# Kernel tuning notes

Measured on AMD Instinct MI355X. Metric: run time of the kernel, lower is better.

Reference implementation:

```python
import jax, jax.numpy as jnp
import numpy as np

DT = 0.1
N_STEPS = 20
STEP_SIZE = DT / N_STEPS


def setup_inputs() -> dict:
    key = jax.random.key(0)
    ks = jax.random.split(key, 8)
    sizes = [1024, 2048, 2048, 10]
    batch = 4096
    inp = {
        "x": jax.random.uniform(ks[0], (batch, sizes[0]), dtype=jnp.float32),
        "w0": jax.random.normal(ks[1], (sizes[0], sizes[1]), dtype=jnp.float32) / np.sqrt(sizes[0]),
        "w1": jax.random.normal(ks[2], (sizes[1], sizes[2]), dtype=jnp.float32) / np.sqrt(sizes[1]),
        "w2": jax.random.normal(ks[3], (sizes[2], sizes[3]), dtype=jnp.float32) / np.sqrt(sizes[2]),
        "b0": jnp.zeros((sizes[1],), jnp.float32),
        "b1": jnp.zeros((sizes[2],), jnp.float32),
        "b2": jnp.zeros((sizes[3],), jnp.float32),
        "s1": jax.random.uniform(ks[4], (batch, sizes[1]), dtype=jnp.float32),
        "s2": jax.random.uniform(ks[5], (batch, sizes[2]), dtype=jnp.float32),
        "s3": jax.random.uniform(ks[6], (batch, sizes[3]), dtype=jnp.float32),
    }
    return inp


def reference(x, w0, w1, w2, b0, b1, b2, s1, s2, s3):
    weights = [w0, w1, w2]
    biases = [b0, b1, b2]
    sig = jax.nn.sigmoid

    def dsig(v):
        s = sig(v)
        return s * (1.0 - s)

    def body(states, _):
        st = list(states)  # [s0(=x, clamped), s1, s2, s3]
        # hidden layers (indices 1..len-2), sequential in-place semantics
        for i in range(1, 3):
            pre = sig(st[i - 1]) @ weights[i - 1] + sig(st[i + 1]) @ weights[i].T + biases[i - 1]
            grad = dsig(st[i]) * pre - st[i]
            st[i] = st[i] - STEP_SIZE * grad
        # output layer (no target / beta=0 in eval mode)
        grad = dsig(st[3]) * (sig(st[2]) @ weights[2] + biases[2]) - st[3]
        st[3] = st[3] - STEP_SIZE * grad
        return tuple(st), None

    init = (x, s1, s2, s3)
    final, _ = jax.lax.scan(body, init, None, length=N_STEPS)
    return final[-1]
```

## Files before the change

### kernel.cpp

```cpp
#include <hip/hip_runtime.h>
#include <cstdint>
#include <cstddef>

using u16 = unsigned short;
using u32 = unsigned int;

typedef __bf16 bf16x8 __attribute__((ext_vector_type(8)));
typedef float f32x4 __attribute__((ext_vector_type(4)));
typedef u16 u16x4 __attribute__((ext_vector_type(4)));

#define DEV __device__ __forceinline__

constexpr float SS = 0.1f / 20.0f;

DEV float sigm(float x) { return 1.0f / (1.0f + __expf(-x)); }

DEV u16 f2bf(float f) {
  union { float f; u32 u; } v; v.f = f;
  u32 r = v.u + 0x7FFFu + ((v.u >> 16) & 1u);
  return (u16)(r >> 16);
}
DEV float bf2f(u16 h) {
  union { u32 u; float f; } v; v.u = ((u32)h) << 16;
  return v.f;
}

__global__ void k_prep(const float* __restrict__ in, float* __restrict__ fcopy,
                       float* __restrict__ sigf32, u16* __restrict__ sigb,
                       u16* __restrict__ rawb, int n) {
  int stride = gridDim.x * blockDim.x;
  for (int i = blockIdx.x * blockDim.x + threadIdx.x; i < n; i += stride) {
    float v = in[i];
    if (fcopy) fcopy[i] = v;
    if (rawb) rawb[i] = f2bf(v);
    if (sigf32 || sigb) {
      float s = sigm(v);
      if (sigf32) sigf32[i] = s;
      if (sigb) sigb[i] = f2bf(s);
    }
  }
}

__global__ void k_transpose_bf16(const float* __restrict__ in, u16* __restrict__ out,
                                 int K, int N) {
  __shared__ float tile[32][33];
  int kb = blockIdx.x * 32, nb = blockIdx.y * 32;
  int tx = threadIdx.x & 31, ty = threadIdx.x >> 5;
#pragma unroll
  for (int i = 0; i < 4; ++i)
    tile[ty + 8 * i][tx] = in[(size_t)(kb + ty + 8 * i) * N + nb + tx];
  __syncthreads();
#pragma unroll
  for (int i = 0; i < 4; ++i)
    out[(size_t)(nb + ty + 8 * i) * K + kb + tx] = f2bf(tile[tx][ty + 8 * i]);
}

template <int MODE>
__launch_bounds__(256)
__global__ void k_gemm(const u16* __restrict__ A, const u16* __restrict__ Bt,
                       int M, int N, int K,
                       const u16* __restrict__ addcb, const float* __restrict__ bias,
                       const float* __restrict__ sig3, const float* __restrict__ w2,
                       float* __restrict__ statef, u16* __restrict__ sigb) {
  constexpr int BM = 128, BN = 128, BK = 64;
  __shared__ __align__(16) u16 Als[2][BM * BK];
  __shared__ __align__(16) u16 Bls[2][BN * BK];
  int b = blockIdx.x;
  int xcd = b & 7, slot = b >> 3;
  int tm = ((((xcd >> 1) << 3) | (slot >> 3))) * BM;
  int tn = ((((xcd & 1) << 3) | (slot & 7))) * BN;
  int tid = threadIdx.x;
  int lane = tid & 63, wid = tid >> 6;
  int l15 = lane & 15, lhi = lane >> 4;
  int wm = (wid >> 1) * 64, wn = (wid & 1) * 64;

  const u16* Ag = A + (size_t)tm * K;
  const u16* Bg = Bt + (size_t)tn * K;

  f32x4 acc[4][4] = {};

  auto stage = [&](int buf, int k0) {
#pragma unroll
    for (int rd = 0; rd < 4; ++rd) {
      int S = rd * 256 + tid;
      int row = S >> 3;
      int cs = ((S & 7) ^ (row & 7)) * 8;
      __builtin_amdgcn_global_load_lds(
          (const __attribute__((address_space(1))) u32*)(Ag + (size_t)row * K + k0 + cs),
          (__attribute__((address_space(3))) u32*)(&Als[buf][0] + S * 8), 16, 0, 0);
      __builtin_amdgcn_global_load_lds(
          (const __attribute__((address_space(1))) u32*)(Bg + (size_t)row * K + k0 + cs),
          (__attribute__((address_space(3))) u32*)(&Bls[buf][0] + S * 8), 16, 0, 0);
    }
  };

  auto compute = [&](int buf) {
    __builtin_amdgcn_s_setprio(1);
#pragma unroll
    for (int s = 0; s < 2; ++s) {
      bf16x8 af[4], bfr[4];
#pragma unroll
      for (int i = 0; i < 4; ++i) {
        int row = wm + i * 16 + l15;
        af[i] = *(const bf16x8*)(&Als[buf][0] + row * BK + (((s * 4 + lhi) ^ (row & 7)) * 8));
      }
#pragma unroll
      for (int j = 0; j < 4; ++j) {
        int row = wn + j * 16 + l15;
        bfr[j] = *(const bf16x8*)(&Bls[buf][0] + row * BK + (((s * 4 + lhi) ^ (row & 7)) * 8));
      }
#pragma unroll
      for (int i = 0; i < 4; ++i)
#pragma unroll
        for (int j = 0; j < 4; ++j)
          acc[i][j] = __builtin_amdgcn_mfma_f32_16x16x32_bf16(bfr[j], af[i], acc[i][j], 0, 0, 0);
    }
    __builtin_amdgcn_s_setprio(0);
  };

  const int nt = K / BK;
  stage(0, 0);
  stage(1, BK);
  asm volatile("s_waitcnt vmcnt(8)" ::: "memory");
  __builtin_amdgcn_s_barrier();
  asm volatile("" ::: "memory");

  int t = 0;
  for (; t + 3 < nt; t += 2) {
    compute(0);
    asm volatile("" ::: "memory");
    __builtin_amdgcn_s_barrier();
    asm volatile("" ::: "memory");
    stage(0, (t + 2) * BK);
    asm volatile("s_waitcnt vmcnt(8)" ::: "memory");
    __builtin_amdgcn_s_barrier();
    asm volatile("" ::: "memory");

    compute(1);
    asm volatile("" ::: "memory");
    __builtin_amdgcn_s_barrier();
    asm volatile("" ::: "memory");
    stage(1, (t + 3) * BK);
    asm volatile("s_waitcnt vmcnt(8)" ::: "memory");
    __builtin_amdgcn_s_barrier();
    asm volatile("" ::: "memory");
  }
  compute(0);
  asm volatile("s_waitcnt vmcnt(0)" ::: "memory");
  __builtin_amdgcn_s_barrier();
  asm volatile("" ::: "memory");
  compute(1);

  if constexpr (MODE == 0) {
#pragma unroll
    for (int i = 0; i < 4; ++i) {
      int gr = tm + wm + i * 16 + l15;
#pragma unroll
      for (int j = 0; j < 4; ++j) {
        int gc0 = tn + wn + j * 16 + 4 * lhi;
        u16x4 sb;
#pragma unroll
        for (int rr = 0; rr < 4; ++rr) sb[rr] = f2bf(acc[i][j][rr] + bias[gc0 + rr]);
        *(u16x4*)(sigb + (size_t)gr * N + gc0) = sb;
      }
    }
  } else if constexpr (MODE == 1) {
#pragma unroll
    for (int i = 0; i < 4; ++i) {
      int gr = tm + wm + i * 16 + l15;
#pragma unroll
      for (int j = 0; j < 4; ++j) {
        int gc0 = tn + wn + j * 16 + 4 * lhi;
        size_t idx = (size_t)gr * N + gc0;
        u16x4 ab = *(const u16x4*)(addcb + idx);
        f32x4 old = *(const f32x4*)(statef + idx);
        f32x4 nv; u16x4 sb;
#pragma unroll
        for (int rr = 0; rr < 4; ++rr) {
          float pre = acc[i][j][rr] + bf2f(ab[rr]);
          float o = old[rr];
          float sg = sigm(o);
          float n = o - SS * (sg * (1.0f - sg) * pre - o);
          nv[rr] = n; sb[rr] = f2bf(sigm(n));
        }
        *(f32x4*)(statef + idx) = nv;
        *(u16x4*)(sigb + idx) = sb;
      }
    }
  } else {
    float s3v[4][10];
#pragma unroll
    for (int i = 0; i < 4; ++i) {
      int gr = tm + wm + i * 16 + l15;
#pragma unroll
      for (int k = 0; k < 10; ++k) s3v[i][k] = sig3[gr * 10 + k];
    }
#pragma unroll
    for (int j = 0; j < 4; ++j) {
      int gc0 = tn + wn + j * 16 + 4 * lhi;
      float wv[4][10]; f32x4 bb;
#pragma unroll
      for (int rr = 0; rr < 4; ++rr) {
        bb[rr] = bias[gc0 + rr];
#pragma unroll
        for (int k = 0; k < 10; ++k) wv[rr][k] = w2[(gc0 + rr) * 10 + k];
      }
#pragma unroll
      for (int i = 0; i < 4; ++i) {
        int gr = tm + wm + i * 16 + l15;
        size_t idx = (size_t)gr * N + gc0;
        f32x4 old = *(const f32x4*)(statef + idx);
        f32x4 nv; u16x4 sb;
#pragma unroll
        for (int rr = 0; rr < 4; ++rr) {
          float ex = bb[rr];
#pragma unroll
          for (int k = 0; k < 10; ++k) ex += s3v[i][k] * wv[rr][k];
          float pre = acc[i][j][rr] + ex;
          float o = old[rr];
          float sg = sigm(o);
          float n = o - SS * (sg * (1.0f - sg) * pre - o);
          nv[rr] = n; sb[rr] = f2bf(sigm(n));
        }
        *(f32x4*)(statef + idx) = nv;
        *(u16x4*)(sigb + idx) = sb;
      }
    }
  }
}

__global__ void k_out(const u16* __restrict__ sigs2b, const float* __restrict__ w2,
                      const float* __restrict__ b2, float* __restrict__ s3f,
                      float* __restrict__ sigs3f, float* __restrict__ outOrNull) {
  int tid = threadIdx.x;
  int r = tid >> 4, l16 = tid & 15;
  int row = blockIdx.x * 16 + r;
  float acc[10] = {};
  const u16* arow = sigs2b + (size_t)row * 2048;
  for (int kb = l16; kb < 256; kb += 16) {
    u16x4 v0 = *(const u16x4*)(arow + kb * 8);
    u16x4 v1 = *(const u16x4*)(arow + kb * 8 + 4);
    float a[8];
#pragma unroll
    for (int e = 0; e < 4; ++e) { a[e] = bf2f(v0[e]); a[e + 4] = bf2f(v1[e]); }
    const float* wr = w2 + (size_t)kb * 80;
#pragma unroll
    for (int e = 0; e < 8; ++e)
#pragma unroll
      for (int n = 0; n < 10; ++n) acc[n] += a[e] * wr[e * 10 + n];
  }
#pragma unroll
  for (int m = 1; m < 16; m <<= 1)
#pragma unroll
    for (int n = 0; n < 10; ++n) acc[n] += __shfl_xor(acc[n], m, 64);
  if (l16 < 10) {
    float pre = 0.0f;
#pragma unroll
    for (int n = 0; n < 10; ++n)
      if (l16 == n) pre = acc[n];
    pre += b2[l16];
    size_t idx = (size_t)row * 10 + l16;
    float old = s3f[idx];
    float sg = sigm(old);
    float nv = old - SS * (sg * (1.0f - sg) * pre - old);
    s3f[idx] = nv;
    sigs3f[idx] = sigm(nv);
    if (outOrNull) outOrNull[idx] = nv;
  }
}

extern "C" void kernel_launch(void* const* d_in, const int* in_sizes, int n_in,
                              void* d_out, int out_size, void* d_ws, size_t ws_size,
                              hipStream_t stream) {
  const float* x  = (const float*)d_in[0];
  const float* w0 = (const float*)d_in[1];
  const float* w1 = (const float*)d_in[2];
  const float* w2 = (const float*)d_in[3];
  const float* b0 = (const float*)d_in[4];
  const float* b1 = (const float*)d_in[5];
  const float* b2 = (const float*)d_in[6];
  const float* s1 = (const float*)d_in[7];
  const float* s2 = (const float*)d_in[8];
  const float* s3 = (const float*)d_in[9];
  float* out = (float*)d_out;

  uint8_t* p = (uint8_t*)d_ws;
  auto alloc = [&](size_t bytes) {
    uint8_t* r = p;
    p += (bytes + 255) & ~(size_t)255;
    return r;
  };
  float* s1f    = (float*)alloc(4096ull * 2048 * 4);
  float* s2f    = (float*)alloc(4096ull * 2048 * 4);
  u16*   addcb  = (u16*)alloc(4096ull * 2048 * 2);
  u16*   sigs1b = (u16*)alloc(4096ull * 2048 * 2);
  u16*   sigs2b = (u16*)alloc(4096ull * 2048 * 2);
  u16*   sigxb  = (u16*)alloc(4096ull * 1024 * 2);
  u16*   w1b    = (u16*)alloc(2048ull * 2048 * 2);
  u16*   w1tb   = (u16*)alloc(2048ull * 2048 * 2);
  u16*   w0tb   = (u16*)alloc(2048ull * 1024 * 2);
  float* s3f    = (float*)alloc(4096ull * 10 * 4);
  float* sigs3f = (float*)alloc(4096ull * 10 * 4);
  (void)ws_size; (void)in_sizes; (void)n_in; (void)out_size;

  auto grid = [](int n) { int g = (n + 255) / 256; return g > 2048 ? 2048 : g; };

  k_prep<<<grid(4096 * 1024), 256, 0, stream>>>(x, nullptr, nullptr, sigxb, nullptr, 4096 * 1024);
  k_prep<<<grid(2048 * 2048), 256, 0, stream>>>(w1, nullptr, nullptr, nullptr, w1b, 2048 * 2048);
  k_prep<<<grid(4096 * 2048), 256, 0, stream>>>(s1, s1f, nullptr, nullptr, nullptr, 4096 * 2048);
  k_prep<<<grid(4096 * 2048), 256, 0, stream>>>(s2, s2f, nullptr, sigs2b, nullptr, 4096 * 2048);
  k_prep<<<grid(40960), 256, 0, stream>>>(s3, s3f, sigs3f, nullptr, nullptr, 40960);
  k_transpose_bf16<<<dim3(1024 / 32, 2048 / 32), 256, 0, stream>>>(w0, w0tb, 1024, 2048);
  k_transpose_bf16<<<dim3(2048 / 32, 2048 / 32), 256, 0, stream>>>(w1, w1tb, 2048, 2048);

  k_gemm<0><<<512, 256, 0, stream>>>(sigxb, w0tb, 4096, 2048, 1024,
                                     nullptr, b0, nullptr, nullptr, nullptr, addcb);

  for (int t = 0; t < 20; ++t) {
    k_gemm<1><<<512, 256, 0, stream>>>(sigs2b, w1b, 4096, 2048, 2048,
                                       addcb, nullptr, nullptr, nullptr, s1f, sigs1b);
    k_gemm<2><<<512, 256, 0, stream>>>(sigs1b, w1tb, 4096, 2048, 2048,
                                       nullptr, b1, sigs3f, w2, s2f, sigs2b);
    k_out<<<256, 256, 0, stream>>>(sigs2b, w2, b2, s3f, sigs3f, (t == 19) ? out : nullptr);
  }
}
```

Measured before the change: 2.521 ms.

## Use 8-wave GEMM blocks and store fp32 state in per-thread swizzled layout

```diff
diff --git a/kernel.cpp b/kernel.cpp
--- a/kernel.cpp
+++ b/kernel.cpp
@@ -55,8 +55,31 @@
     out[(size_t)(nb + ty + 8 * i) * K + kb + tx] = f2bf(tile[tx][ty + 8 * i]);
 }
 
+DEV void tile_base(int b, int& tm, int& tn) {
+  int xcd = b & 7, slot = b >> 3;
+  tm = ((((xcd >> 1) << 3) | (slot >> 3))) * 128;
+  tn = ((((xcd & 1) << 3) | (slot & 7))) * 128;
+}
+
+__global__ void k_init_state(const float* __restrict__ src, float* __restrict__ dst_swz) {
+  int b = blockIdx.x;
+  int tm, tn; tile_base(b, tm, tn);
+  int tid = threadIdx.x, lane = tid & 63, wid = tid >> 6;
+  int l15 = lane & 15, lhi = lane >> 4;
+  int wm = (wid >> 2) * 64, wn = (wid & 3) * 32;
+#pragma unroll
+  for (int i = 0; i < 4; ++i)
+#pragma unroll
+    for (int j = 0; j < 2; ++j) {
+      int gr = tm + wm + i * 16 + l15;
+      int gc0 = tn + wn + j * 16 + 4 * lhi;
+      f32x4 v = *(const f32x4*)(src + (size_t)gr * 2048 + gc0);
+      *(f32x4*)(dst_swz + (((size_t)b * 8 + i * 2 + j) * 512 + tid) * 4) = v;
+    }
+}
+
 template <int MODE>
-__launch_bounds__(256)
+__launch_bounds__(512, 4)
 __global__ void k_gemm(const u16* __restrict__ A, const u16* __restrict__ Bt,
                        int M, int N, int K,
                        const u16* __restrict__ addcb, const float* __restrict__ bias,
@@ -66,23 +89,21 @@
   __shared__ __align__(16) u16 Als[2][BM * BK];
   __shared__ __align__(16) u16 Bls[2][BN * BK];
   int b = blockIdx.x;
-  int xcd = b & 7, slot = b >> 3;
-  int tm = ((((xcd >> 1) << 3) | (slot >> 3))) * BM;
-  int tn = ((((xcd & 1) << 3) | (slot & 7))) * BN;
+  int tm, tn; tile_base(b, tm, tn);
   int tid = threadIdx.x;
   int lane = tid & 63, wid = tid >> 6;
   int l15 = lane & 15, lhi = lane >> 4;
-  int wm = (wid >> 1) * 64, wn = (wid & 1) * 64;
+  int wm = (wid >> 2) * 64, wn = (wid & 3) * 32;
 
   const u16* Ag = A + (size_t)tm * K;
   const u16* Bg = Bt + (size_t)tn * K;
 
-  f32x4 acc[4][4] = {};
+  f32x4 acc[4][2] = {};
 
   auto stage = [&](int buf, int k0) {
 #pragma unroll
-    for (int rd = 0; rd < 4; ++rd) {
-      int S = rd * 256 + tid;
+    for (int rd = 0; rd < 2; ++rd) {
+      int S = rd * 512 + tid;
       int row = S >> 3;
       int cs = ((S & 7) ^ (row & 7)) * 8;
       __builtin_amdgcn_global_load_lds(
@@ -98,21 +119,21 @@
     __builtin_amdgcn_s_setprio(1);
 #pragma unroll
     for (int s = 0; s < 2; ++s) {
-      bf16x8 af[4], bfr[4];
+      bf16x8 af[4], bfr[2];
 #pragma unroll
       for (int i = 0; i < 4; ++i) {
         int row = wm + i * 16 + l15;
         af[i] = *(const bf16x8*)(&Als[buf][0] + row * BK + (((s * 4 + lhi) ^ (row & 7)) * 8));
       }
 #pragma unroll
-      for (int j = 0; j < 4; ++j) {
+      for (int j = 0; j < 2; ++j) {
         int row = wn + j * 16 + l15;
         bfr[j] = *(const bf16x8*)(&Bls[buf][0] + row * BK + (((s * 4 + lhi) ^ (row & 7)) * 8));
       }
 #pragma unroll
       for (int i = 0; i < 4; ++i)
 #pragma unroll
-        for (int j = 0; j < 4; ++j)
+        for (int j = 0; j < 2; ++j)
           acc[i][j] = __builtin_amdgcn_mfma_f32_16x16x32_bf16(bfr[j], af[i], acc[i][j], 0, 0, 0);
     }
     __builtin_amdgcn_s_setprio(0);
@@ -121,7 +142,7 @@
   const int nt = K / BK;
   stage(0, 0);
   stage(1, BK);
-  asm volatile("s_waitcnt vmcnt(8)" ::: "memory");
+  asm volatile("s_waitcnt vmcnt(4)" ::: "memory");
   __builtin_amdgcn_s_barrier();
   asm volatile("" ::: "memory");
 
@@ -132,7 +153,7 @@
     __builtin_amdgcn_s_barrier();
     asm volatile("" ::: "memory");
     stage(0, (t + 2) * BK);
-    asm volatile("s_waitcnt vmcnt(8)" ::: "memory");
+    asm volatile("s_waitcnt vmcnt(4)" ::: "memory");
     __builtin_amdgcn_s_barrier();
     asm volatile("" ::: "memory");
 
@@ -141,7 +162,7 @@
     __builtin_amdgcn_s_barrier();
     asm volatile("" ::: "memory");
     stage(1, (t + 3) * BK);
-    asm volatile("s_waitcnt vmcnt(8)" ::: "memory");
+    asm volatile("s_waitcnt vmcnt(4)" ::: "memory");
     __builtin_amdgcn_s_barrier();
     asm volatile("" ::: "memory");
   }
@@ -153,27 +174,26 @@
 
   if constexpr (MODE == 0) {
 #pragma unroll
-    for (int i = 0; i < 4; ++i) {
-      int gr = tm + wm + i * 16 + l15;
-#pragma unroll
-      for (int j = 0; j < 4; ++j) {
+    for (int i = 0; i < 4; ++i)
+#pragma unroll
+      for (int j = 0; j < 2; ++j) {
         int gc0 = tn + wn + j * 16 + 4 * lhi;
+        size_t sidx = (((size_t)b * 8 + i * 2 + j) * 512 + tid) * 4;
         u16x4 sb;
 #pragma unroll
         for (int rr = 0; rr < 4; ++rr) sb[rr] = f2bf(acc[i][j][rr] + bias[gc0 + rr]);
-        *(u16x4*)(sigb + (size_t)gr * N + gc0) = sb;
-      }
-    }
+        *(u16x4*)(sigb + sidx) = sb;
+      }
   } else if constexpr (MODE == 1) {
 #pragma unroll
-    for (int i = 0; i < 4; ++i) {
-      int gr = tm + wm + i * 16 + l15;
-#pragma unroll
-      for (int j = 0; j < 4; ++j) {
+    for (int i = 0; i < 4; ++i)
+#pragma unroll
+      for (int j = 0; j < 2; ++j) {
+        int gr = tm + wm + i * 16 + l15;
         int gc0 = tn + wn + j * 16 + 4 * lhi;
-        size_t idx = (size_t)gr * N + gc0;
-        u16x4 ab = *(const u16x4*)(addcb + idx);
-        f32x4 old = *(const f32x4*)(statef + idx);
+        size_t sidx = (((size_t)b * 8 + i * 2 + j) * 512 + tid) * 4;
+        u16x4 ab = *(const u16x4*)(addcb + sidx);
+        f32x4 old = *(const f32x4*)(statef + sidx);
         f32x4 nv; u16x4 sb;
 #pragma unroll
         for (int rr = 0; rr < 4; ++rr) {
@@ -183,10 +203,9 @@
           float n = o - SS * (sg * (1.0f - sg) * pre - o);
           nv[rr] = n; sb[rr] = f2bf(sigm(n));
         }
-        *(f32x4*)(statef + idx) = nv;
-        *(u16x4*)(sigb + idx) = sb;
-      }
-    }
+        *(f32x4*)(statef + sidx) = nv;
+        *(u16x4*)(sigb + (size_t)gr * N + gc0) = sb;
+      }
   } else {
     float s3v[4][10];
 #pragma unroll
@@ -196,7 +215,7 @@
       for (int k = 0; k < 10; ++k) s3v[i][k] = sig3[gr * 10 + k];
     }
 #pragma unroll
-    for (int j = 0; j < 4; ++j) {
+    for (int j = 0; j < 2; ++j) {
       int gc0 = tn + wn + j * 16 + 4 * lhi;
       float wv[4][10]; f32x4 bb;
 #pragma unroll
@@ -208,8 +227,8 @@
 #pragma unroll
       for (int i = 0; i < 4; ++i) {
         int gr = tm + wm + i * 16 + l15;
-        size_t idx = (size_t)gr * N + gc0;
-        f32x4 old = *(const f32x4*)(statef + idx);
+        size_t sidx = (((size_t)b * 8 + i * 2 + j) * 512 + tid) * 4;
+        f32x4 old = *(const f32x4*)(statef + sidx);
         f32x4 nv; u16x4 sb;
 #pragma unroll
         for (int rr = 0; rr < 4; ++rr) {
@@ -222,8 +241,8 @@
           float n = o - SS * (sg * (1.0f - sg) * pre - o);
           nv[rr] = n; sb[rr] = f2bf(sigm(n));
         }
-        *(f32x4*)(statef + idx) = nv;
-        *(u16x4*)(sigb + idx) = sb;
+        *(f32x4*)(statef + sidx) = nv;
+        *(u16x4*)(sigb + (size_t)gr * N + gc0) = sb;
       }
     }
   }
@@ -307,19 +326,20 @@
 
   k_prep<<<grid(4096 * 1024), 256, 0, stream>>>(x, nullptr, nullptr, sigxb, nullptr, 4096 * 1024);
   k_prep<<<grid(2048 * 2048), 256, 0, stream>>>(w1, nullptr, nullptr, nullptr, w1b, 2048 * 2048);
-  k_prep<<<grid(4096 * 2048), 256, 0, stream>>>(s1, s1f, nullptr, nullptr, nullptr, 4096 * 2048);
-  k_prep<<<grid(4096 * 2048), 256, 0, stream>>>(s2, s2f, nullptr, sigs2b, nullptr, 4096 * 2048);
+  k_prep<<<grid(4096 * 2048), 256, 0, stream>>>(s2, nullptr, nullptr, sigs2b, nullptr, 4096 * 2048);
   k_prep<<<grid(40960), 256, 0, stream>>>(s3, s3f, sigs3f, nullptr, nullptr, 40960);
+  k_init_state<<<512, 512, 0, stream>>>(s1, s1f);
+  k_init_state<<<512, 512, 0, stream>>>(s2, s2f);
   k_transpose_bf16<<<dim3(1024 / 32, 2048 / 32), 256, 0, stream>>>(w0, w0tb, 1024, 2048);
   k_transpose_bf16<<<dim3(2048 / 32, 2048 / 32), 256, 0, stream>>>(w1, w1tb, 2048, 2048);
 
-  k_gemm<0><<<512, 256, 0, stream>>>(sigxb, w0tb, 4096, 2048, 1024,
+  k_gemm<0><<<512, 512, 0, stream>>>(sigxb, w0tb, 4096, 2048, 1024,
                                      nullptr, b0, nullptr, nullptr, nullptr, addcb);
 
   for (int t = 0; t < 20; ++t) {
-    k_gemm<1><<<512, 256, 0, stream>>>(sigs2b, w1b, 4096, 2048, 2048,
+    k_gemm<1><<<512, 512, 0, stream>>>(sigs2b, w1b, 4096, 2048, 2048,
                                        addcb, nullptr, nullptr, nullptr, s1f, sigs1b);
-    k_gemm<2><<<512, 256, 0, stream>>>(sigs1b, w1tb, 4096, 2048, 2048,
+    k_gemm<2><<<512, 512, 0, stream>>>(sigs1b, w1tb, 4096, 2048, 2048,
                                        nullptr, b1, sigs3f, w2, s2f, sigs2b);
     k_out<<<256, 256, 0, stream>>>(sigs2b, w2, b2, s3f, sigs3f, (t == 19) ? out : nullptr);
   }
```

Result: no change. 2.503 ms (median of 2 runs) (-0.8%).
